# Performance work log

Hardware: AMD Instinct MI355X
Metric: run time of the kernel (lower is better)

The kernel has to match this reference:

```python
import jax, jax.numpy as jnp
import numpy as np

NEG_BIG = -9e15
LRELU_SLOPE = 0.2  # torch LeakyReLU default used for act_att


def setup_inputs() -> dict:
    key = jax.random.key(0)
    k1, k2, k3, k4 = jax.random.split(key, 4)
    B, N, F_in, F_out = 8, 2048, 128, 64
    inp = jax.random.normal(k1, (B, N, F_in), dtype=jnp.float32)
    adj = jax.random.randint(k2, (N, N), 0, 2, dtype=jnp.int32)
    W = jax.random.normal(k3, (F_in, F_out), dtype=jnp.float32) * (1.0 / np.sqrt(F_in))
    a = jax.random.normal(k4, (2 * F_out, 1), dtype=jnp.float32) * (1.0 / np.sqrt(2 * F_out))
    return {"input": inp, "adj": adj, "W": W, "a": a}


def reference(input, adj, W, a):
    # h: [B, N, F_out]
    h = jnp.einsum('bnf,fo->bno', input, W)
    F_out = W.shape[1]
    a1 = a[:F_out, 0]   # [F_out] -- applied to source node i
    a2 = a[F_out:, 0]   # [F_out] -- applied to target node j
    # e[b,i,j] = leaky_relu(h_i . a1 + h_j . a2); equivalent to cat([h_i,h_j]) @ a
    s1 = h @ a1          # [B, N]
    s2 = h @ a2          # [B, N]
    e = jax.nn.leaky_relu(s1[:, :, None] + s2[:, None, :], negative_slope=LRELU_SLOPE)
    masked = jnp.where(adj[None, :, :] > 0, e, NEG_BIG)
    attention = jax.nn.softmax(masked, axis=-1)  # [B, N, N]
    # dropout p=0.0 (eval) -> identity
    h_prime = jnp.einsum('bij,bjo->bio', attention, h)
    out = jax.nn.relu(h_prime)  # concat=True -> apply act_gat
    return out, attention[..., None]
```

## Files before the change

### kernel.cpp

```cpp
#include <hip/hip_runtime.h>
#include <hip/hip_bf16.h>

constexpr int B = 8, N = 2048, FIN = 128, FOUT = 64;

typedef __attribute__((ext_vector_type(8))) short short8;
typedef __attribute__((ext_vector_type(4))) float f32x4;

__device__ __forceinline__ unsigned int pk_bf16(float lo, float hi) {
    union { __hip_bfloat162 h2; unsigned int u; } c;
    c.h2 = __float22bfloat162_rn(float2{lo, hi});
    return c.u;
}
__device__ __forceinline__ unsigned short f2bf(float f) {
    return (unsigned short)(pk_bf16(f, 0.f) & 0xFFFFu);
}

__global__ __launch_bounds__(512, 2) void kA(
        const float* __restrict__ inp, const float* __restrict__ W,
        const float* __restrict__ a, const int* __restrict__ adj,
        unsigned short* __restrict__ hP, float* __restrict__ s1,
        float* __restrict__ s2, unsigned long long* __restrict__ adjbits) {
    __shared__ float wa1l[128], wa2l[128];
    __shared__ unsigned short wT[64][136];
    __shared__ unsigned short aT[128][136];

    int bx = blockIdx.x, t = threadIdx.x, w = t >> 6, lane = t & 63;

    if (bx >= 128) {
        int row = (bx - 128) * 8 + w;
        const int* ar = adj + (size_t)row * N;
        unsigned long long* br = adjbits + (size_t)row * 32;
        #pragma unroll 8
        for (int wq = 0; wq < 32; ++wq) {
            unsigned long long m = __ballot(ar[wq * 64 + lane] > 0);
            if (lane == 0) br[wq] = m;
        }
        return;
    }

    int b = bx >> 4, i0 = (bx & 15) * 128;

    if (t < 128) {
        const float* wr = W + t * FOUT;
        float acc1 = 0.f;
        #pragma unroll 16
        for (int o = 0; o < 64; ++o) acc1 = fmaf(wr[o], a[o], acc1);
        wa1l[t] = acc1;
    } else if (t < 256) {
        int k = t - 128;
        const float* wr = W + k * FOUT;
        float acc2 = 0.f;
        #pragma unroll 16
        for (int o = 0; o < 64; ++o) acc2 = fmaf(wr[o], a[64 + o], acc2);
        wa2l[k] = acc2;
    } else {
        int t2 = t - 256;
        int o = t2 & 63, kg = t2 >> 6;
        #pragma unroll 8
        for (int kk = 0; kk < 32; ++kk) {
            int k = kg * 32 + kk;
            wT[o][k] = f2bf(W[k * FOUT + o]);
        }
    }
    __syncthreads();

    {
        int row = t >> 2, seg = t & 3;
        const float* ip = inp + ((size_t)b * N + i0 + row) * FIN + seg * 32;
        float s1p = 0.f, s2p = 0.f;
        #pragma unroll
        for (int q = 0; q < 8; ++q) {
            float4 v = *(const float4*)&ip[q * 4];
            int k = seg * 32 + q * 4;
            s1p += v.x * wa1l[k] + v.y * wa1l[k + 1] + v.z * wa1l[k + 2] + v.w * wa1l[k + 3];
            s2p += v.x * wa2l[k] + v.y * wa2l[k + 1] + v.z * wa2l[k + 2] + v.w * wa2l[k + 3];
            unsigned int* dst = (unsigned int*)&aT[row][k];
            dst[0] = pk_bf16(v.x, v.y);
            dst[1] = pk_bf16(v.z, v.w);
        }
        s1p += __shfl_xor(s1p, 1); s1p += __shfl_xor(s1p, 2);
        s2p += __shfl_xor(s2p, 1); s2p += __shfl_xor(s2p, 2);
        if (seg == 0) {
            s1[(size_t)b * N + i0 + row] = s1p;
            s2[(size_t)b * N + i0 + row] = s2p;
        }
    }
    __syncthreads();

    int r = lane & 15, g = lane >> 4;
    int mloc = w * 16;
    f32x4 acc[4];
    #pragma unroll
    for (int nf = 0; nf < 4; ++nf)
        #pragma unroll
        for (int q = 0; q < 4; ++q) acc[nf][q] = 0.f;
    #pragma unroll
    for (int ks = 0; ks < 4; ++ks) {
        short8 Af = *(const short8*)&aT[mloc + r][ks * 32 + g * 8];
        #pragma unroll
        for (int nf = 0; nf < 4; ++nf) {
            short8 Bf = *(const short8*)&wT[nf * 16 + r][ks * 32 + g * 8];
            acc[nf] = __builtin_amdgcn_mfma_f32_16x16x32_bf16(Af, Bf, acc[nf], 0, 0, 0);
        }
    }
    __syncthreads();

    #pragma unroll
    for (int nf = 0; nf < 4; ++nf)
        #pragma unroll
        for (int q = 0; q < 4; ++q)
            aT[mloc + g * 4 + q][nf * 16 + r] = f2bf(acc[nf][q]);
    __syncthreads();

    #pragma unroll
    for (int half = 0; half < 2; ++half) {
        int idx = t + half * 512;
        int kb_l = idx >> 8, nf = (idx >> 6) & 3, ln = idx & 63;
        int g2 = ln >> 4, r2 = ln & 15;
        union { short8 s8; unsigned short u[8]; } tw;
        #pragma unroll
        for (int e = 0; e < 8; ++e)
            tw.u[e] = aT[kb_l * 32 + g2 * 8 + e][nf * 16 + r2];
        int kbg = (bx & 15) * 4 + kb_l;
        *(short8*)&hP[((((size_t)b * 64 + kbg) * 4 + nf) << 9) + ln * 8] = tw.s8;
    }
}

__global__ __launch_bounds__(256, 2) void k2_fused(
        const float* __restrict__ s1g, const float* __restrict__ s2g,
        const unsigned long long* __restrict__ adjbits,
        const unsigned short* __restrict__ hP,
        float* __restrict__ att, float* __restrict__ out) {
    __shared__ float s2l[N];
    __shared__ float s1l[16];
    __shared__ float ps[4][16];
    __shared__ float rvl[16];
    __shared__ float red[3][16][68];

    int L = blockIdx.x;
    int b = L & 7, m0 = (L >> 3) * 16;
    int t = threadIdx.x, kc = t >> 6, lane = t & 63;
    int r = lane & 15, g = lane >> 4;

    {
        int j = t * 8;
        *(float4*)&s2l[j]     = *(const float4*)&s2g[(size_t)b * N + j];
        *(float4*)&s2l[j + 4] = *(const float4*)&s2g[(size_t)b * N + j + 4];
    }
    if (t < 16) s1l[t] = s1g[(size_t)b * N + m0 + t];
    __syncthreads();

    float s1v = s1l[r];
    const unsigned long long* brow = adjbits + (size_t)(m0 + r) * 32 + kc * 8;
    const unsigned short* hpb = hP + (size_t)b * 64 * 4 * 512;

    f32x4 acc[4];
    #pragma unroll
    for (int nf = 0; nf < 4; ++nf)
        #pragma unroll
        for (int q = 0; q < 4; ++q) acc[nf][q] = 0.f;
    float rsum = 0.f;

    #pragma unroll 1
    for (int so = 0; so < 4; ++so) {
        unsigned long long bw0 = brow[so * 2];
        unsigned long long bw1 = brow[so * 2 + 1];
        #pragma unroll
        for (int si = 0; si < 4; ++si) {
            int st = so * 4 + si;
            int jb = kc * 512 + st * 32 + g * 8;
            unsigned long long bwv = (si < 2) ? bw0 : bw1;
            unsigned int bits = (unsigned int)(bwv >> ((si & 1) * 32 + g * 8)) & 0xFFu;
            float4 sA = *(const float4*)&s2l[jb];
            float4 sB = *(const float4*)&s2l[jb + 4];
            union { short8 s8; unsigned int d[4]; } pk;
            {
                float xa, xb, pa, pb;
                xa = s1v + sA.x; xa = fmaxf(xa, 0.2f * xa);
                xb = s1v + sA.y; xb = fmaxf(xb, 0.2f * xb);
                pa = (bits & 1u) ? __expf(xa) : 0.f;
                pb = (bits & 2u) ? __expf(xb) : 0.f;
                rsum += pa + pb; pk.d[0] = pk_bf16(pa, pb);
                xa = s1v + sA.z; xa = fmaxf(xa, 0.2f * xa);
                xb = s1v + sA.w; xb = fmaxf(xb, 0.2f * xb);
                pa = (bits & 4u) ? __expf(xa) : 0.f;
                pb = (bits & 8u) ? __expf(xb) : 0.f;
                rsum += pa + pb; pk.d[1] = pk_bf16(pa, pb);
                xa = s1v + sB.x; xa = fmaxf(xa, 0.2f * xa);
                xb = s1v + sB.y; xb = fmaxf(xb, 0.2f * xb);
                pa = (bits & 16u) ? __expf(xa) : 0.f;
                pb = (bits & 32u) ? __expf(xb) : 0.f;
                rsum += pa + pb; pk.d[2] = pk_bf16(pa, pb);
                xa = s1v + sB.z; xa = fmaxf(xa, 0.2f * xa);
                xb = s1v + sB.w; xb = fmaxf(xb, 0.2f * xb);
                pa = (bits & 64u) ? __expf(xa) : 0.f;
                pb = (bits & 128u) ? __expf(xb) : 0.f;
                rsum += pa + pb; pk.d[3] = pk_bf16(pa, pb);
            }
            int kb = kc * 16 + st;
            const unsigned short* hs = hpb + (((size_t)kb * 4) << 9) + lane * 8;
            #pragma unroll
            for (int nf = 0; nf < 4; ++nf) {
                short8 Bf = *(const short8*)&hs[nf << 9];
                acc[nf] = __builtin_amdgcn_mfma_f32_16x16x32_bf16(pk.s8, Bf, acc[nf], 0, 0, 0);
            }
        }
    }
    rsum += __shfl_xor(rsum, 16);
    rsum += __shfl_xor(rsum, 32);
    if (lane < 16) ps[kc][r] = rsum;
    if (kc > 0) {
        #pragma unroll
        for (int nf = 0; nf < 4; ++nf)
            #pragma unroll
            for (int q = 0; q < 4; ++q)
                red[kc - 1][4 * g + q][nf * 16 + r] = acc[nf][q];
    }
    __syncthreads();
    if (t < 16)
        rvl[t] = 1.0f / (ps[0][t] + ps[1][t] + ps[2][t] + ps[3][t]);
    __syncthreads();

    if (kc == 0) {
        #pragma unroll
        for (int nf = 0; nf < 4; ++nf) {
            #pragma unroll
            for (int q = 0; q < 4; ++q) {
                int m = 4 * g + q;
                int o = nf * 16 + r;
                float vv = acc[nf][q] + red[0][m][o] + red[1][m][o] + red[2][m][o];
                vv *= rvl[m];
                out[((size_t)b * N + m0 + m) * FOUT + o] = vv > 0.f ? vv : 0.f;
            }
        }
    }

    #pragma unroll
    for (int rr = 0; rr < 4; ++rr) {
        int row = kc * 4 + rr;
        float s1r = s1l[row];
        float rvr = rvl[row];
        const unsigned long long* br2 = adjbits + (size_t)(m0 + row) * 32;
        float* orow = att + ((size_t)b * N + m0 + row) * N;
        #pragma unroll
        for (int it = 0; it < 8; ++it) {
            int j = it * 256 + lane * 4;
            unsigned int bits = (unsigned int)(br2[j >> 6] >> (j & 63)) & 0xFu;
            float4 sv = *(const float4*)&s2l[j];
            float x0 = s1r + sv.x; x0 = fmaxf(x0, 0.2f * x0);
            float x1 = s1r + sv.y; x1 = fmaxf(x1, 0.2f * x1);
            float x2 = s1r + sv.z; x2 = fmaxf(x2, 0.2f * x2);
            float x3 = s1r + sv.w; x3 = fmaxf(x3, 0.2f * x3);
            float4 o;
            o.x = (bits & 1u) ? __expf(x0) * rvr : 0.f;
            o.y = (bits & 2u) ? __expf(x1) * rvr : 0.f;
            o.z = (bits & 4u) ? __expf(x2) * rvr : 0.f;
            o.w = (bits & 8u) ? __expf(x3) * rvr : 0.f;
            *(float4*)&orow[j] = o;
        }
    }
}

extern "C" void kernel_launch(void* const* d_in, const int* in_sizes, int n_in,
                              void* d_out, int out_size, void* d_ws, size_t ws_size,
                              hipStream_t stream) {
    const float* inp = (const float*)d_in[0];
    const int*   adj = (const int*)d_in[1];
    const float* W   = (const float*)d_in[2];
    const float* a   = (const float*)d_in[3];

    float* out = (float*)d_out;
    float* att = out + (size_t)B * N * FOUT;

    unsigned short* hP = (unsigned short*)d_ws;
    float* s1  = (float*)(hP + (size_t)B * FOUT * N);
    float* s2  = s1 + (size_t)B * N;
    unsigned long long* adjbits = (unsigned long long*)(s2 + (size_t)B * N);

    kA<<<384, 512, 0, stream>>>(inp, W, a, adj, hP, s1, s2, adjbits);
    k2_fused<<<1024, 256, 0, stream>>>(s1, s2, adjbits, hP, att, out);
}
```

Baseline: 53.26 us.

## Precompute softmax row sums and fuse normalized attention stores into MFMA loop

```diff
diff --git a/kernel.cpp b/kernel.cpp
--- a/kernel.cpp
+++ b/kernel.cpp
@@ -133,7 +133,6 @@
         float* __restrict__ att, float* __restrict__ out) {
     __shared__ float s2l[N];
     __shared__ float s1l[16];
-    __shared__ float ps[4][16];
     __shared__ float rvl[16];
     __shared__ float red[3][16][68];
 
@@ -150,16 +149,43 @@
     if (t < 16) s1l[t] = s1g[(size_t)b * N + m0 + t];
     __syncthreads();
 
+    #pragma unroll
+    for (int rr = 0; rr < 4; ++rr) {
+        int row = kc * 4 + rr;
+        float s1r = s1l[row];
+        const unsigned long long* br2 = adjbits + (size_t)(m0 + row) * 32;
+        float rsum = 0.f;
+        #pragma unroll
+        for (int it = 0; it < 8; ++it) {
+            int j = it * 256 + lane * 4;
+            unsigned int bits = (unsigned int)(br2[j >> 6] >> (j & 63)) & 0xFu;
+            float4 sv = *(const float4*)&s2l[j];
+            float x0 = s1r + sv.x; x0 = fmaxf(x0, 0.2f * x0);
+            float x1 = s1r + sv.y; x1 = fmaxf(x1, 0.2f * x1);
+            float x2 = s1r + sv.z; x2 = fmaxf(x2, 0.2f * x2);
+            float x3 = s1r + sv.w; x3 = fmaxf(x3, 0.2f * x3);
+            rsum += (bits & 1u) ? __expf(x0) : 0.f;
+            rsum += (bits & 2u) ? __expf(x1) : 0.f;
+            rsum += (bits & 4u) ? __expf(x2) : 0.f;
+            rsum += (bits & 8u) ? __expf(x3) : 0.f;
+        }
+        #pragma unroll
+        for (int off = 1; off < 64; off <<= 1) rsum += __shfl_xor(rsum, off);
+        if (lane == 0) rvl[row] = 1.0f / rsum;
+    }
+    __syncthreads();
+
     float s1v = s1l[r];
+    float rvv = rvl[r];
     const unsigned long long* brow = adjbits + (size_t)(m0 + r) * 32 + kc * 8;
     const unsigned short* hpb = hP + (size_t)b * 64 * 4 * 512;
+    float* attrow = att + ((size_t)b * N + m0 + r) * N;
 
     f32x4 acc[4];
     #pragma unroll
     for (int nf = 0; nf < 4; ++nf)
         #pragma unroll
         for (int q = 0; q < 4; ++q) acc[nf][q] = 0.f;
-    float rsum = 0.f;
 
     #pragma unroll 1
     for (int so = 0; so < 4; ++so) {
@@ -174,29 +200,32 @@
             float4 sA = *(const float4*)&s2l[jb];
             float4 sB = *(const float4*)&s2l[jb + 4];
             union { short8 s8; unsigned int d[4]; } pk;
+            float4 o0, o1;
             {
                 float xa, xb, pa, pb;
                 xa = s1v + sA.x; xa = fmaxf(xa, 0.2f * xa);
                 xb = s1v + sA.y; xb = fmaxf(xb, 0.2f * xb);
-                pa = (bits & 1u) ? __expf(xa) : 0.f;
-                pb = (bits & 2u) ? __expf(xb) : 0.f;
-                rsum += pa + pb; pk.d[0] = pk_bf16(pa, pb);
+                pa = (bits & 1u) ? __expf(xa) * rvv : 0.f;
+                pb = (bits & 2u) ? __expf(xb) * rvv : 0.f;
+                o0.x = pa; o0.y = pb; pk.d[0] = pk_bf16(pa, pb);
                 xa = s1v + sA.z; xa = fmaxf(xa, 0.2f * xa);
                 xb = s1v + sA.w; xb = fmaxf(xb, 0.2f * xb);
-                pa = (bits & 4u) ? __expf(xa) : 0.f;
-                pb = (bits & 8u) ? __expf(xb) : 0.f;
-                rsum += pa + pb; pk.d[1] = pk_bf16(pa, pb);
+                pa = (bits & 4u) ? __expf(xa) * rvv : 0.f;
+                pb = (bits & 8u) ? __expf(xb) * rvv : 0.f;
+                o0.z = pa; o0.w = pb; pk.d[1] = pk_bf16(pa, pb);
                 xa = s1v + sB.x; xa = fmaxf(xa, 0.2f * xa);
                 xb = s1v + sB.y; xb = fmaxf(xb, 0.2f * xb);
-                pa = (bits & 16u) ? __expf(xa) : 0.f;
-                pb = (bits & 32u) ? __expf(xb) : 0.f;
-                rsum += pa + pb; pk.d[2] = pk_bf16(pa, pb);
+                pa = (bits & 16u) ? __expf(xa) * rvv : 0.f;
+                pb = (bits & 32u) ? __expf(xb) * rvv : 0.f;
+                o1.x = pa; o1.y = pb; pk.d[2] = pk_bf16(pa, pb);
                 xa = s1v + sB.z; xa = fmaxf(xa, 0.2f * xa);
                 xb = s1v + sB.w; xb = fmaxf(xb, 0.2f * xb);
-                pa = (bits & 64u) ? __expf(xa) : 0.f;
-                pb = (bits & 128u) ? __expf(xb) : 0.f;
-                rsum += pa + pb; pk.d[3] = pk_bf16(pa, pb);
+                pa = (bits & 64u) ? __expf(xa) * rvv : 0.f;
+                pb = (bits & 128u) ? __expf(xb) * rvv : 0.f;
+                o1.z = pa; o1.w = pb; pk.d[3] = pk_bf16(pa, pb);
             }
+            *(float4*)&attrow[jb]     = o0;
+            *(float4*)&attrow[jb + 4] = o1;
             int kb = kc * 16 + st;
             const unsigned short* hs = hpb + (((size_t)kb * 4) << 9) + lane * 8;
             #pragma unroll
@@ -206,9 +235,6 @@
             }
         }
     }
-    rsum += __shfl_xor(rsum, 16);
-    rsum += __shfl_xor(rsum, 32);
-    if (lane < 16) ps[kc][r] = rsum;
     if (kc > 0) {
         #pragma unroll
         for (int nf = 0; nf < 4; ++nf)
@@ -217,10 +243,6 @@
                 red[kc - 1][4 * g + q][nf * 16 + r] = acc[nf][q];
     }
     __syncthreads();
-    if (t < 16)
-        rvl[t] = 1.0f / (ps[0][t] + ps[1][t] + ps[2][t] + ps[3][t]);
-    __syncthreads();
-
     if (kc == 0) {
         #pragma unroll
         for (int nf = 0; nf < 4; ++nf) {
@@ -229,34 +251,8 @@
                 int m = 4 * g + q;
                 int o = nf * 16 + r;
                 float vv = acc[nf][q] + red[0][m][o] + red[1][m][o] + red[2][m][o];
-                vv *= rvl[m];
                 out[((size_t)b * N + m0 + m) * FOUT + o] = vv > 0.f ? vv : 0.f;
             }
-        }
-    }
-
-    #pragma unroll
-    for (int rr = 0; rr < 4; ++rr) {
-        int row = kc * 4 + rr;
-        float s1r = s1l[row];
-        float rvr = rvl[row];
-        const unsigned long long* br2 = adjbits + (size_t)(m0 + row) * 32;
-        float* orow = att + ((size_t)b * N + m0 + row) * N;
-        #pragma unroll
-        for (int it = 0; it < 8; ++it) {
-            int j = it * 256 + lane * 4;
-            unsigned int bits = (unsigned int)(br2[j >> 6] >> (j & 63)) & 0xFu;
-            float4 sv = *(const float4*)&s2l[j];
-            float x0 = s1r + sv.x; x0 = fmaxf(x0, 0.2f * x0);
-            float x1 = s1r + sv.y; x1 = fmaxf(x1, 0.2f * x1);
-            float x2 = s1r + sv.z; x2 = fmaxf(x2, 0.2f * x2);
-            float x3 = s1r + sv.w; x3 = fmaxf(x3, 0.2f * x3);
-            float4 o;
-            o.x = (bits & 1u) ? __expf(x0) * rvr : 0.f;
-            o.y = (bits & 2u) ? __expf(x1) * rvr : 0.f;
-            o.z = (bits & 4u) ? __expf(x2) * rvr : 0.f;
-            o.w = (bits & 8u) ? __expf(x3) * rvr : 0.f;
-            *(float4*)&orow[j] = o;
         }
     }
 }
```

Result: slower. 62.68 us (+17.7%).
